# Performance work log

Hardware: AMD Instinct MI355X
Metric: run time of the kernel (lower is better)

The kernel has to match this reference:

```python
import jax, jax.numpy as jnp
import numpy as np
from jax import lax

N = 16384          # num_nodes (LSTM sequence length, batch=1)
AVG_DEG = 32
E_EDGES = N * AVG_DEG
FEAT = 512         # cmd_args.feat_dim (tag vocab)
EMB = 256          # embedding_size -> LSTM input = 2*EMB
H = 512            # LSTM hidden_size
MLP_H = 512        # cmd_args.hidden
C = 10             # cmd_args.num_class


def setup_inputs() -> dict:
    key = jax.random.key(0)
    ks = jax.random.split(key, 14)
    s = 1.0 / np.sqrt(H)
    u = lambda k, shape: jax.random.uniform(k, shape, jnp.float32, -s, s)
    return {
        "node_tags": jax.random.randint(ks[0], (N,), 0, FEAT),
        "neighbor_node_ids": jax.random.randint(ks[1], (E_EDGES,), 0, N),
        "neighbor_tag_ids": jax.random.randint(ks[2], (E_EDGES,), 0, FEAT),
        "label": jax.random.randint(ks[3], (1,), 0, C),
        "W_emb": u(ks[4], (FEAT, EMB)),
        "b_emb": u(ks[5], (EMB,)),
        "W_ih": u(ks[6], (4 * H, 2 * EMB)),  # torch LSTM gate order: i, f, g, o
        "W_hh": u(ks[7], (4 * H, H)),
        "b_lstm": u(ks[8], (4 * H,)),        # b_ih + b_hh folded together
        "W1": u(ks[9], (H, MLP_H)),
        "b1": u(ks[10], (MLP_H,)),
        "W2": u(ks[11], (MLP_H, C)),
        "b2": u(ks[12], (C,)),
    }


def reference(node_tags, neighbor_node_ids, neighbor_tag_ids, label,
              W_emb, b_emb, W_ih, W_hh, b_lstm, W1, b1, W2, b2):
    n = node_tags.shape[0]
    feat_dim = W_emb.shape[0]
    hid = W_hh.shape[1]

    # one-hot(node_tags) @ W_emb + b  ==  row-gather of W_emb
    node_emb = W_emb[node_tags] + b_emb                      # [N, EMB]

    # ragged neighbor-tag histogram via scatter-add (the Python double loop)
    hist = jnp.zeros((n, feat_dim), dtype=W_emb.dtype)
    hist = hist.at[neighbor_node_ids, neighbor_tag_ids].add(1.0)  # [N, FEAT]
    nb_emb = hist @ W_emb + b_emb                            # [N, EMB]

    x = jnp.concatenate([node_emb, nb_emb], axis=1)          # [N, 2*EMB]

    # single-layer LSTM, batch=1, seq_len=N; precompute input projections
    pre = x @ W_ih.T + b_lstm                                # [N, 4H]

    def step(carry, p):
        h, c = carry
        g = p + h @ W_hh.T                                   # [4H]
        i, f, gg, o = jnp.split(g, 4)
        i = jax.nn.sigmoid(i)
        f = jax.nn.sigmoid(f)
        o = jax.nn.sigmoid(o)
        c = f * c + i * jnp.tanh(gg)
        h = o * jnp.tanh(c)
        return (h, c), h

    init = (jnp.zeros((hid,), x.dtype), jnp.zeros((hid,), x.dtype))
    _, hs = lax.scan(step, init, pre)                        # hs: [N, H]

    embed = jnp.sum(hs, axis=0)[None, :]                     # [1, H] (sum over time)

    # MLPClassifier: Linear -> ReLU -> Linear -> log_softmax
    h1 = jax.nn.relu(embed @ W1 + b1)
    logits = h1 @ W2 + b2                                    # [1, C]
    return jax.nn.log_softmax(logits, axis=-1)
```

## Files before the change

### kernel.cpp

```cpp
#include <hip/hip_runtime.h>
#include <hip/hip_bf16.h>

#define N_NODES 16384
#define E_EDGESN (16384*32)
#define FEAT 512
#define EMB 256
#define HID 512
#define G4 2048
#define XDIM 512
#define NWG 32
#define UPW 16
#define NREP 4
#define REPW 4096

typedef __attribute__((ext_vector_type(8))) short bf16x8;
typedef __attribute__((ext_vector_type(4))) float f32x4;

__device__ __forceinline__ float b2f(unsigned short u) {
  union { unsigned int i; float f; } v; v.i = ((unsigned int)u) << 16; return v.f;
}
__device__ __forceinline__ unsigned short f2b(float f) {
  union { float f; unsigned int i; } v; v.f = f;
  unsigned int x = v.i;
  unsigned int r = (x + 0x7FFFu + ((x >> 16) & 1u)) >> 16;
  return (unsigned short)r;
}
__device__ __forceinline__ float fast_sigmoid(float x) {
  return __builtin_amdgcn_rcpf(1.0f + __expf(-x));
}
__device__ __forceinline__ float fast_tanh(float x) {
  return fmaf(-2.0f, __builtin_amdgcn_rcpf(1.0f + __expf(2.0f * x)), 1.0f);
}

__global__ __launch_bounds__(256) void k_detect(const unsigned* __restrict__ w,
                                                unsigned* __restrict__ flag) {
  __shared__ int cnt;
  if (threadIdx.x == 0) cnt = 0;
  __syncthreads();
  int hits = 0;
#pragma unroll
  for (int j = 0; j < 4; ++j) {
    unsigned wv = w[threadIdx.x * 4 + j];
    unsigned e = (wv >> 7) & 0xFFu;
    if ((e >= 90u && e <= 126u) || ((wv & 0xFFFFu) == 0u)) hits++;
  }
  atomicAdd(&cnt, hits);
  __syncthreads();
  if (threadIdx.x == 0) *flag = (cnt < 512) ? 1u : 0u;
}

__global__ void k_convert(const void* __restrict__ src, unsigned short* __restrict__ dst,
                          int n, const unsigned* __restrict__ flag) {
  int i = blockIdx.x * blockDim.x + threadIdx.x;
  if (i >= n) return;
  if (*flag) dst[i] = f2b(((const float*)src)[i]);
  else       dst[i] = ((const unsigned short*)src)[i];
}

__global__ void k_hist(const int* __restrict__ nid, const int* __restrict__ ntag,
                       unsigned* __restrict__ hist) {
  int e = blockIdx.x * blockDim.x + threadIdx.x;
  if (e < E_EDGESN)
    atomicAdd(&hist[(size_t)nid[e] * FEAT + ntag[e]], 1u);
}

__global__ __launch_bounds__(256) void k_build_x(
    const int* __restrict__ tags, const unsigned* __restrict__ hist,
    const unsigned short* __restrict__ Wemb, const unsigned short* __restrict__ bemb,
    unsigned short* __restrict__ x) {
  __shared__ int f_lds[160];
  __shared__ float c_lds[160];
  __shared__ int nlist;
  int n = blockIdx.x, c = threadIdx.x;
  if (c == 0) nlist = 0;
  __syncthreads();
  for (int f = c; f < FEAT; f += 256) {
    unsigned cnt = hist[(size_t)n * FEAT + f];
    if (cnt) {
      int idx = atomicAdd(&nlist, 1);
      if (idx < 160) { f_lds[idx] = f; c_lds[idx] = (float)cnt; }
    }
  }
  __syncthreads();
  int m = nlist; if (m > 160) m = 160;
  float be = b2f(bemb[c]);
  int tg = tags[n];
  x[(size_t)n * XDIM + c] = f2b(b2f(Wemb[(size_t)tg * EMB + c]) + be);
  float acc = be;
  for (int j = 0; j < m; ++j)
    acc += c_lds[j] * b2f(Wemb[(size_t)f_lds[j] * EMB + c]);
  x[(size_t)n * XDIM + EMB + c] = f2b(acc);
}

__global__ __launch_bounds__(256) void k_gemm_pre(
    const unsigned short* __restrict__ x, const unsigned short* __restrict__ Wih,
    const unsigned short* __restrict__ blstm, unsigned short* __restrict__ pre) {
  int wave = threadIdx.x >> 6, lane = threadIdx.x & 63;
  int row = lane & 15, quad = lane >> 4;
  int mband = blockIdx.y * 64 + wave * 16;
  int nbase = blockIdx.x * 128;
  f32x4 acc[8] = {};
  const unsigned short* ap = x + (size_t)(mband + row) * XDIM + quad * 8;
  const unsigned short* bp0 = Wih + (size_t)(nbase + row) * XDIM + quad * 8;
  for (int kc = 0; kc < 16; ++kc) {
    bf16x8 af = *(const bf16x8*)(ap + kc * 32);
#pragma unroll
    for (int nt = 0; nt < 8; ++nt) {
      bf16x8 bf = *(const bf16x8*)(bp0 + (size_t)nt * 16 * XDIM + kc * 32);
      acc[nt] = __builtin_amdgcn_mfma_f32_16x16x32_bf16(af, bf, acc[nt], 0, 0, 0);
    }
  }
#pragma unroll
  for (int nt = 0; nt < 8; ++nt) {
    int nn = nbase + nt * 16 + row;
    float bv = b2f(blstm[nn]);
    int pn = ((nn & 511) << 2) | (nn >> 9);
#pragma unroll
    for (int i = 0; i < 4; ++i) {
      int mm = mband + quad * 4 + i;
      pre[(size_t)mm * G4 + pn] = f2b(acc[nt][i] + bv);
    }
  }
}

__global__ __launch_bounds__(256, 1) void k_scan(
    const unsigned short* __restrict__ Whh, const unsigned short* __restrict__ prep,
    unsigned* __restrict__ hw, float* __restrict__ embed) {
  __shared__ float h_lds[HID];
  int tid = threadIdx.x, wg = blockIdx.x;
  int ug = tid >> 4;
  int s  = tid & 15;
  int lane = tid & 63;
  int unit = wg * UPW + ug;

  float wreg[4][32];
#pragma unroll
  for (int g = 0; g < 4; ++g) {
    const unsigned* wp = (const unsigned*)(Whh + (size_t)(g * HID + unit) * HID);
#pragma unroll
    for (int j = 0; j < 16; ++j) {
      unsigned wv = wp[16 * j + s];
      wreg[g][2 * j]     = b2f((unsigned short)(wv & 0xFFFFu));
      wreg[g][2 * j + 1] = b2f((unsigned short)(wv >> 16));
    }
  }

  unsigned pc0[8], pc1[8];
  if (s == 4) {
#pragma unroll
    for (int i = 0; i < 8; ++i) {
      const unsigned* pp = (const unsigned*)(prep + (size_t)i * G4 + (unsigned)unit * 4u);
      pc0[i] = pp[0]; pc1[i] = pp[1];
    }
  }
  int bsrc = (lane & 48) | 4;

  float cstate = 0.0f, eacc = 0.0f;
  h_lds[tid] = 0.0f;
  h_lds[256 + tid] = 0.0f;
  __syncthreads();

  unsigned myrep = (unsigned)(wg & (NREP - 1));

  for (int t = 0; t < N_NODES; ++t) {
    float a0 = 0.f, a1 = 0.f, a2 = 0.f, a3 = 0.f;
    const float2* hb = (const float2*)h_lds;
#pragma unroll
    for (int j = 0; j < 16; ++j) {
      float2 hv = hb[j * 16 + s];
      a0 += wreg[0][2*j] * hv.x + wreg[0][2*j+1] * hv.y;
      a1 += wreg[1][2*j] * hv.x + wreg[1][2*j+1] * hv.y;
      a2 += wreg[2][2*j] * hv.x + wreg[2][2*j+1] * hv.y;
      a3 += wreg[3][2*j] * hv.x + wreg[3][2*j+1] * hv.y;
    }
#pragma unroll
    for (int off = 1; off < 16; off <<= 1) {
      a0 += __shfl_xor(a0, off);
      a1 += __shfl_xor(a1, off);
      a2 += __shfl_xor(a2, off);
      a3 += __shfl_xor(a3, off);
    }

    unsigned w0 = __shfl(pc0[t & 7], bsrc, 64);
    unsigned w1 = __shfl(pc1[t & 7], bsrc, 64);

    float gi = fast_sigmoid(a0 + b2f((unsigned short)(w0 & 0xFFFFu)));
    float gf = fast_sigmoid(a1 + b2f((unsigned short)(w0 >> 16)));
    float gg = fast_tanh   (a2 + b2f((unsigned short)(w1 & 0xFFFFu)));
    float go = fast_sigmoid(a3 + b2f((unsigned short)(w1 >> 16)));
    cstate = gf * cstate + gi * gg;
    float hn = go * fast_tanh(cstate);
    if (s == 0) eacc += hn;

    unsigned tagw = (unsigned)t & 0xFFu;
    if (t < N_NODES - 1) {
      union { float f; unsigned u; } cu; cu.f = hn;
      unsigned word = (cu.u & 0xFFFFFF00u) | tagw;
      unsigned slotw = ((unsigned)t & 1u) << 9;
      if (s == 0) {
        __hip_atomic_store(&hw[0 * REPW + slotw + unit], word,
                           __ATOMIC_RELAXED, __HIP_MEMORY_SCOPE_AGENT);
        __hip_atomic_store(&hw[1 * REPW + slotw + unit], word,
                           __ATOMIC_RELAXED, __HIP_MEMORY_SCOPE_AGENT);
      } else if (s == 8) {
        __hip_atomic_store(&hw[2 * REPW + slotw + unit], word,
                           __ATOMIC_RELAXED, __HIP_MEMORY_SCOPE_AGENT);
        __hip_atomic_store(&hw[3 * REPW + slotw + unit], word,
                           __ATOMIC_RELAXED, __HIP_MEMORY_SCOPE_AGENT);
      }
    }
    if (s == 4 && (t & 7) == 7) {
#pragma unroll
      for (int i = 0; i < 8; ++i) {
        int row = t + 1 + i;
        if (row >= N_NODES) row = 0;
        const unsigned* pp = (const unsigned*)(prep + (size_t)row * G4 + (unsigned)unit * 4u);
        pc0[i] = pp[0]; pc1[i] = pp[1];
      }
    }

    if (t < N_NODES - 1) {
      unsigned long long* qp = (unsigned long long*)
          (hw + myrep * REPW + (((unsigned)t & 1u) << 9)) + tid;
      unsigned v0, v1;
      int tries = 0;
      for (;;) {
        unsigned long long v = __hip_atomic_load(qp, __ATOMIC_RELAXED,
                                                 __HIP_MEMORY_SCOPE_AGENT);
        v0 = (unsigned)v; v1 = (unsigned)(v >> 32);
        if ((((v0 ^ tagw) | (v1 ^ tagw)) & 0xFFu) == 0u) break;
        if (++tries > 128) __builtin_amdgcn_s_sleep(1);
      }
      h_lds[2 * tid]     = __uint_as_float(v0 & 0xFFFFFF00u);
      h_lds[2 * tid + 1] = __uint_as_float(v1 & 0xFFFFFF00u);
      __syncthreads();
    }
  }
  if (s == 0) embed[unit] = eacc;
}

__global__ __launch_bounds__(512) void k_head(
    const float* __restrict__ embed, const unsigned short* __restrict__ W1,
    const unsigned short* __restrict__ b1, const unsigned short* __restrict__ W2,
    const unsigned short* __restrict__ b2, void* __restrict__ out,
    const unsigned* __restrict__ flag) {
  __shared__ float e_s[HID], h1_s[HID];
  __shared__ float lg[16];
  int tid = threadIdx.x;
  e_s[tid] = embed[tid];
  __syncthreads();
  float sum = b2f(b1[tid]);
  for (int i = 0; i < HID; ++i)
    sum += e_s[i] * b2f(W1[(size_t)i * HID + tid]);
  h1_s[tid] = fmaxf(sum, 0.0f);
  __syncthreads();
  if (tid < 10) {
    float l = b2f(b2[tid]);
    for (int j = 0; j < HID; ++j)
      l += h1_s[j] * b2f(W2[(size_t)j * 10 + tid]);
    lg[tid] = l;
  }
  __syncthreads();
  if (tid == 0) {
    float m = -1e30f;
    for (int c = 0; c < 10; ++c) m = fmaxf(m, lg[c]);
    float se = 0.f;
    for (int c = 0; c < 10; ++c) se += expf(lg[c] - m);
    float lse = m + logf(se);
    if (*flag) {
      for (int c = 0; c < 10; ++c) ((float*)out)[c] = lg[c] - lse;
    } else {
      for (int c = 0; c < 10; ++c) ((unsigned short*)out)[c] = f2b(lg[c] - lse);
    }
  }
}

extern "C" void kernel_launch(void* const* d_in, const int* in_sizes, int n_in,
                              void* d_out, int out_size, void* d_ws, size_t ws_size,
                              hipStream_t stream) {
  const int* node_tags = (const int*)d_in[0];
  const int* nid = (const int*)d_in[1];
  const int* ntag = (const int*)d_in[2];

  char* ws = (char*)d_ws;
  unsigned short* pre  = (unsigned short*)ws;
  unsigned short* x    = (unsigned short*)(ws + 67108864);
  unsigned*       hist = (unsigned*)(ws + 83886080);
  char* tail = ws + 117440512;
  unsigned* hw    = (unsigned*)tail;
  unsigned* flag  = (unsigned*)(tail + 65536);
  float*    embed = (float*)(tail + 65792);
  char* wc = tail + 69632;
  unsigned short* Wemb_c  = (unsigned short*)(wc);
  unsigned short* bemb_c  = (unsigned short*)(wc + 262144);
  unsigned short* Wih_c   = (unsigned short*)(wc + 262656);
  unsigned short* Whh_c   = (unsigned short*)(wc + 2359808);
  unsigned short* blstm_c = (unsigned short*)(wc + 4456960);
  unsigned short* W1_c    = (unsigned short*)(wc + 4461056);
  unsigned short* b1_c    = (unsigned short*)(wc + 4985344);
  unsigned short* W2_c    = (unsigned short*)(wc + 4986368);
  unsigned short* b2_c    = (unsigned short*)(wc + 4996608);

  hipMemsetAsync(hist, 0, 33554432, stream);

  k_detect<<<1, 256, 0, stream>>>((const unsigned*)d_in[6], flag);

  struct { const void* s; unsigned short* d; int n; } cv[9] = {
    { d_in[4],  Wemb_c,  FEAT * EMB },
    { d_in[5],  bemb_c,  EMB },
    { d_in[6],  Wih_c,   G4 * XDIM },
    { d_in[7],  Whh_c,   G4 * HID },
    { d_in[8],  blstm_c, G4 },
    { d_in[9],  W1_c,    HID * HID },
    { d_in[10], b1_c,    HID },
    { d_in[11], W2_c,    HID * 10 },
    { d_in[12], b2_c,    10 },
  };
  for (int i = 0; i < 9; ++i)
    k_convert<<<(cv[i].n + 255) / 256, 256, 0, stream>>>(cv[i].s, cv[i].d, cv[i].n, flag);

  k_hist<<<E_EDGESN / 256, 256, 0, stream>>>(nid, ntag, hist);
  k_build_x<<<N_NODES, 256, 0, stream>>>(node_tags, hist, Wemb_c, bemb_c, x);
  k_gemm_pre<<<dim3(G4 / 128, N_NODES / 64), 256, 0, stream>>>(x, Wih_c, blstm_c, pre);
  k_scan<<<NWG, 256, 0, stream>>>(Whh_c, pre, hw, embed);
  k_head<<<1, 512, 0, stream>>>(embed, W1_c, b1_c, W2_c, b2_c, d_out, flag);
}
```

Baseline: 29.88 ms.

## Split LSTM scan into 128 single-wave workgroups to drop block barriers

Reworks the persistent LSTM recurrence kernel from 32 workgroups of 256 threads to 128 single-wavefront workgroups handling 4 hidden units each. Because each workgroup is one wave, the per-step __syncthreads is removed, and each lane now polls 4 words of the published hidden state instead of 1. The number of replicated hidden-state buffers grows from 4 to 8 to spread polling traffic, and the per-step gate pre-activations are staged through LDS instead of shuffled from a register array. The trade-off is more workgroups taking part in the cross-workgroup handshake, more global stores per step, and reliance on in-wave ordering for LDS writes and reads without a barrier.

```diff
diff --git a/kernel.cpp b/kernel.cpp
--- a/kernel.cpp
+++ b/kernel.cpp
@@ -8,9 +8,9 @@
 #define HID 512
 #define G4 2048
 #define XDIM 512
-#define NWG 32
-#define UPW 16
-#define NREP 4
+#define NWG 128
+#define UPW 4
+#define NREP 8
 #define REPW 4096
 
 typedef __attribute__((ext_vector_type(8))) short bf16x8;
@@ -123,14 +123,15 @@
   }
 }
 
-__global__ __launch_bounds__(256, 1) void k_scan(
+__global__ __launch_bounds__(64, 1) void k_scan(
     const unsigned short* __restrict__ Whh, const unsigned short* __restrict__ prep,
     unsigned* __restrict__ hw, float* __restrict__ embed) {
   __shared__ float h_lds[HID];
-  int tid = threadIdx.x, wg = blockIdx.x;
-  int ug = tid >> 4;
-  int s  = tid & 15;
-  int lane = tid & 63;
+  __shared__ unsigned pre_s[64];
+  int lane = threadIdx.x;
+  int wg = blockIdx.x;
+  int ug = lane >> 4;
+  int s  = lane & 15;
   int unit = wg * UPW + ug;
 
   float wreg[4][32];
@@ -145,21 +146,16 @@
     }
   }
 
-  unsigned pc0[8], pc1[8];
-  if (s == 4) {
-#pragma unroll
-    for (int i = 0; i < 8; ++i) {
-      const unsigned* pp = (const unsigned*)(prep + (size_t)i * G4 + (unsigned)unit * 4u);
-      pc0[i] = pp[0]; pc1[i] = pp[1];
-    }
-  }
-  int bsrc = (lane & 48) | 4;
+  const unsigned* prep32 = (const unsigned*)prep;
+  if (lane < 32) {
+    int row = lane >> 2;
+    ((unsigned long long*)pre_s)[lane] =
+        *(const unsigned long long*)(prep32 + (size_t)row * 1024 + wg * 8 + 2 * (lane & 3));
+  }
+  ((float4*)h_lds)[lane * 2]     = make_float4(0.f, 0.f, 0.f, 0.f);
+  ((float4*)h_lds)[lane * 2 + 1] = make_float4(0.f, 0.f, 0.f, 0.f);
 
   float cstate = 0.0f, eacc = 0.0f;
-  h_lds[tid] = 0.0f;
-  h_lds[256 + tid] = 0.0f;
-  __syncthreads();
-
   unsigned myrep = (unsigned)(wg & (NREP - 1));
 
   for (int t = 0; t < N_NODES; ++t) {
@@ -181,8 +177,9 @@
       a3 += __shfl_xor(a3, off);
     }
 
-    unsigned w0 = __shfl(pc0[t & 7], bsrc, 64);
-    unsigned w1 = __shfl(pc1[t & 7], bsrc, 64);
+    int p = t & 7;
+    unsigned w0 = pre_s[8 * p + 2 * ug];
+    unsigned w1 = pre_s[8 * p + 2 * ug + 1];
 
     float gi = fast_sigmoid(a0 + b2f((unsigned short)(w0 & 0xFFFFu)));
     float gf = fast_sigmoid(a1 + b2f((unsigned short)(w0 >> 16)));
@@ -192,49 +189,52 @@
     float hn = go * fast_tanh(cstate);
     if (s == 0) eacc += hn;
 
-    unsigned tagw = (unsigned)t & 0xFFu;
+    unsigned long long stg = 0;
+    int do_stage = (p == 7) && (lane < 32);
+    if (do_stage) {
+      int row = t + 1 + (lane >> 2);
+      if (row >= N_NODES) row = 0;
+      stg = *(const unsigned long long*)(prep32 + (size_t)row * 1024 + wg * 8 + 2 * (lane & 3));
+    }
+
     if (t < N_NODES - 1) {
+      unsigned tagw = (unsigned)t & 0xFFu;
+      unsigned slotw = ((unsigned)t & 1u) << 9;
       union { float f; unsigned u; } cu; cu.f = hn;
       unsigned word = (cu.u & 0xFFFFFF00u) | tagw;
-      unsigned slotw = ((unsigned)t & 1u) << 9;
-      if (s == 0) {
-        __hip_atomic_store(&hw[0 * REPW + slotw + unit], word,
+      if (s < 8)
+        __hip_atomic_store(&hw[(unsigned)s * REPW + slotw + (unsigned)unit], word,
                            __ATOMIC_RELAXED, __HIP_MEMORY_SCOPE_AGENT);
-        __hip_atomic_store(&hw[1 * REPW + slotw + unit], word,
-                           __ATOMIC_RELAXED, __HIP_MEMORY_SCOPE_AGENT);
-      } else if (s == 8) {
-        __hip_atomic_store(&hw[2 * REPW + slotw + unit], word,
-                           __ATOMIC_RELAXED, __HIP_MEMORY_SCOPE_AGENT);
-        __hip_atomic_store(&hw[3 * REPW + slotw + unit], word,
-                           __ATOMIC_RELAXED, __HIP_MEMORY_SCOPE_AGENT);
-      }
-    }
-    if (s == 4 && (t & 7) == 7) {
-#pragma unroll
-      for (int i = 0; i < 8; ++i) {
-        int row = t + 1 + i;
-        if (row >= N_NODES) row = 0;
-        const unsigned* pp = (const unsigned*)(prep + (size_t)row * G4 + (unsigned)unit * 4u);
-        pc0[i] = pp[0]; pc1[i] = pp[1];
-      }
-    }
-
-    if (t < N_NODES - 1) {
-      unsigned long long* qp = (unsigned long long*)
-          (hw + myrep * REPW + (((unsigned)t & 1u) << 9)) + tid;
-      unsigned v0, v1;
+
+      unsigned long long* qp =
+          (unsigned long long*)(hw + myrep * REPW + slotw) + lane * 4;
+      unsigned long long tp = (unsigned long long)tagw * 0x0000000100000001ULL;
+      unsigned long long v0, v1, v2, v3;
       int tries = 0;
       for (;;) {
-        unsigned long long v = __hip_atomic_load(qp, __ATOMIC_RELAXED,
-                                                 __HIP_MEMORY_SCOPE_AGENT);
-        v0 = (unsigned)v; v1 = (unsigned)(v >> 32);
-        if ((((v0 ^ tagw) | (v1 ^ tagw)) & 0xFFu) == 0u) break;
-        if (++tries > 128) __builtin_amdgcn_s_sleep(1);
+        v0 = __hip_atomic_load(qp + 0, __ATOMIC_RELAXED, __HIP_MEMORY_SCOPE_AGENT);
+        v1 = __hip_atomic_load(qp + 1, __ATOMIC_RELAXED, __HIP_MEMORY_SCOPE_AGENT);
+        v2 = __hip_atomic_load(qp + 2, __ATOMIC_RELAXED, __HIP_MEMORY_SCOPE_AGENT);
+        v3 = __hip_atomic_load(qp + 3, __ATOMIC_RELAXED, __HIP_MEMORY_SCOPE_AGENT);
+        unsigned long long d = ((v0 ^ tp) | (v1 ^ tp) | (v2 ^ tp) | (v3 ^ tp))
+                               & 0x000000FF000000FFULL;
+        if (d == 0ULL) break;
+        if (++tries > 96) __builtin_amdgcn_s_sleep(1);
       }
-      h_lds[2 * tid]     = __uint_as_float(v0 & 0xFFFFFF00u);
-      h_lds[2 * tid + 1] = __uint_as_float(v1 & 0xFFFFFF00u);
-      __syncthreads();
-    }
+      float4 f0, f1;
+      f0.x = __uint_as_float((unsigned)v0 & 0xFFFFFF00u);
+      f0.y = __uint_as_float((unsigned)(v0 >> 32) & 0xFFFFFF00u);
+      f0.z = __uint_as_float((unsigned)v1 & 0xFFFFFF00u);
+      f0.w = __uint_as_float((unsigned)(v1 >> 32) & 0xFFFFFF00u);
+      f1.x = __uint_as_float((unsigned)v2 & 0xFFFFFF00u);
+      f1.y = __uint_as_float((unsigned)(v2 >> 32) & 0xFFFFFF00u);
+      f1.z = __uint_as_float((unsigned)v3 & 0xFFFFFF00u);
+      f1.w = __uint_as_float((unsigned)(v3 >> 32) & 0xFFFFFF00u);
+      ((float4*)h_lds)[lane * 2]     = f0;
+      ((float4*)h_lds)[lane * 2 + 1] = f1;
+    }
+    if (do_stage)
+      ((unsigned long long*)pre_s)[lane] = stg;
   }
   if (s == 0) embed[unit] = eacc;
 }
@@ -288,9 +288,9 @@
   unsigned*       hist = (unsigned*)(ws + 83886080);
   char* tail = ws + 117440512;
   unsigned* hw    = (unsigned*)tail;
-  unsigned* flag  = (unsigned*)(tail + 65536);
-  float*    embed = (float*)(tail + 65792);
-  char* wc = tail + 69632;
+  unsigned* flag  = (unsigned*)(tail + 131072);
+  float*    embed = (float*)(tail + 131328);
+  char* wc = tail + 135168;
   unsigned short* Wemb_c  = (unsigned short*)(wc);
   unsigned short* bemb_c  = (unsigned short*)(wc + 262144);
   unsigned short* Wih_c   = (unsigned short*)(wc + 262656);
@@ -322,6 +322,6 @@
   k_hist<<<E_EDGESN / 256, 256, 0, stream>>>(nid, ntag, hist);
   k_build_x<<<N_NODES, 256, 0, stream>>>(node_tags, hist, Wemb_c, bemb_c, x);
   k_gemm_pre<<<dim3(G4 / 128, N_NODES / 64), 256, 0, stream>>>(x, Wih_c, blstm_c, pre);
-  k_scan<<<NWG, 256, 0, stream>>>(Whh_c, pre, hw, embed);
+  k_scan<<<NWG, 64, 0, stream>>>(Whh_c, pre, hw, embed);
   k_head<<<1, 512, 0, stream>>>(embed, W1_c, b1_c, W2_c, b2_c, d_out, flag);
 }
```

Measured after the change: 37.55 ms. 25.6% more time.
